# Optimization experiments

Measured on AMD Instinct MI355X. Metric: run time of the kernel, lower is better.

## Reference

```python
import jax, jax.numpy as jnp
import numpy as np

B, T, IN, H = 1024, 128, 5, 100  # batch, seq_len, input_size, hidden_size


def setup_inputs() -> dict:
    key = jax.random.key(0)
    ks = jax.random.split(key, 20)
    bound = 1.0 / np.sqrt(H)  # PyTorch LSTM init: U(-1/sqrt(H), 1/sqrt(H))

    def u(k, shape):
        return jax.random.uniform(k, shape, jnp.float32, -bound, bound)

    inp = {"x": jax.random.normal(ks[0], (B, T, IN), jnp.float32)}
    i = 1
    for layer, din in [(0, IN), (1, 2 * H)]:
        for d in ("f", "b"):
            inp[f"w_ih_l{layer}{d}"] = u(ks[i], (4 * H, din)); i += 1
            inp[f"w_hh_l{layer}{d}"] = u(ks[i], (4 * H, H)); i += 1
            inp[f"b_ih_l{layer}{d}"] = u(ks[i], (4 * H,)); i += 1
            inp[f"b_hh_l{layer}{d}"] = u(ks[i], (4 * H,)); i += 1
    inp["fc_w"] = u(ks[17], (3, 2 * H))
    inp["fc_b"] = u(ks[18], (3,))
    return inp


def _run_dir(x, w_ih, w_hh, b_ih, b_hh, reverse):
    """One LSTM direction. x: [B,T,D] -> hidden seq [B,T,H]. PyTorch gate order i,f,g,o."""
    xT = jnp.swapaxes(x, 0, 1)  # [T,B,D]
    # precompute input contribution for all timesteps: [T,B,4H]
    xg = jnp.einsum('tbd,gd->tbg', xT, w_ih) + b_ih + b_hh

    def step(carry, g_in):
        h, c = carry
        g = g_in + h @ w_hh.T  # [B,4H]
        i, f, gg, o = jnp.split(g, 4, axis=-1)
        c = jax.nn.sigmoid(f) * c + jax.nn.sigmoid(i) * jnp.tanh(gg)
        h = jax.nn.sigmoid(o) * jnp.tanh(c)
        return (h, c), h

    b = x.shape[0]
    init = (jnp.zeros((b, H), x.dtype), jnp.zeros((b, H), x.dtype))
    _, hs = jax.lax.scan(step, init, xg, reverse=reverse)  # hs[t] aligned with time t
    return jnp.swapaxes(hs, 0, 1)  # [B,T,H]


def reference(x,
              w_ih_l0f, w_hh_l0f, b_ih_l0f, b_hh_l0f,
              w_ih_l0b, w_hh_l0b, b_ih_l0b, b_hh_l0b,
              w_ih_l1f, w_hh_l1f, b_ih_l1f, b_hh_l1f,
              w_ih_l1b, w_hh_l1b, b_ih_l1b, b_hh_l1b,
              fc_w, fc_b):
    # Layer 0 (bidirectional): [B,T,2H]
    h0 = jnp.concatenate([
        _run_dir(x, w_ih_l0f, w_hh_l0f, b_ih_l0f, b_hh_l0f, False),
        _run_dir(x, w_ih_l0b, w_hh_l0b, b_ih_l0b, b_hh_l0b, True),
    ], axis=-1)
    # (inter-layer dropout p=0.2 is identity in eval mode)
    # Layer 1 (bidirectional): [B,T,2H]
    h1 = jnp.concatenate([
        _run_dir(h0, w_ih_l1f, w_hh_l1f, b_ih_l1f, b_hh_l1f, False),
        _run_dir(h0, w_ih_l1b, w_hh_l1b, b_ih_l1b, b_hh_l1b, True),
    ], axis=-1)
    last = h1[:, -1, :]  # [B,2H]
    # (dropout p=0.5 is identity in eval mode)
    logits = last @ fc_w.T + fc_b  # [B,3]
    return jax.nn.softmax(logits, axis=1)
```

## Files before the change

kernel.cpp:

```cpp
#include <hip/hip_runtime.h>
#include <hip/hip_fp16.h>


typedef __attribute__((ext_vector_type(8))) short bf16x8;
typedef __attribute__((ext_vector_type(4))) float f32x4;

constexpr int Bsz = 1024, Tt = 128, IN_ = 5, H = 100, G = 400, D1 = 200;
constexpr int NP = 512;
constexpr int NT = 25;
constexpr int MB = 8;
constexpr int MB1 = 4;

__device__ __forceinline__ float sigm(float x)   { return 1.f / (1.f + __expf(-x)); }
__device__ __forceinline__ float tanhf_(float x) { return 1.f - 2.f / (__expf(2.f * x) + 1.f); }
__device__ __forceinline__ unsigned short f2bf(float f) {
  unsigned u = __float_as_uint(f);
  u += 0x7fff + ((u >> 16) & 1);
  return (unsigned short)(u >> 16);
}

__device__ __forceinline__ void pack_body(
    const float* wA, int KA, const float* wB, int KB, int kbo,
    const float* b1, const float* b2, int bias_k,
    unsigned short* dst, int Kg, int idx) {
  if (idx >= Kg * NP * 8) return;
  int jj = idx & 7, rest = idx >> 3;
  int np_ = rest % NP, g = rest / NP;
  int j = np_ >> 2, gate = np_ & 3;
  int k = g * 8 + jj;
  float v = 0.f;
  if (j < H) {
    int n = gate * H + j;
    if (k < KA) v = wA[n * KA + k];
    else if (KB > 0 && k >= kbo && k < kbo + KB) v = wB[n * KB + (k - kbo)];
    else if (k == bias_k) v = b1[n] + b2[n];
  }
  dst[idx] = f2bf(v);
}

__global__ void pack_all(
    const float* __restrict__ w_hh_l0f, const float* __restrict__ w_ih_l0f,
    const float* __restrict__ b_ih_l0f, const float* __restrict__ b_hh_l0f,
    const float* __restrict__ w_hh_l0b, const float* __restrict__ w_ih_l0b,
    const float* __restrict__ b_ih_l0b, const float* __restrict__ b_hh_l0b,
    const float* __restrict__ w_hh_l1f, const float* __restrict__ b_ih_l1f,
    const float* __restrict__ b_hh_l1f,
    const float* __restrict__ w_ih_l1f, const float* __restrict__ w_ih_l1b,
    const float* __restrict__ b_ih_l1b, const float* __restrict__ b_hh_l1b,
    unsigned short* __restrict__ pk0f, unsigned short* __restrict__ pk0b,
    unsigned short* __restrict__ pkhh, unsigned short* __restrict__ pkxg,
    unsigned short* __restrict__ pk1b) {
  int idx = blockIdx.x * 256 + threadIdx.x;
  switch (blockIdx.y) {
    case 0: pack_body(w_hh_l0f, 100, w_ih_l0f, 5, 100, b_ih_l0f, b_hh_l0f, 105, pk0f, 16, idx); break;
    case 1: pack_body(w_hh_l0b, 100, w_ih_l0b, 5, 100, b_ih_l0b, b_hh_l0b, 105, pk0b, 16, idx); break;
    case 2: pack_body(w_hh_l1f, 100, nullptr, 0, 0, b_ih_l1f, b_hh_l1f, -1, pkhh, 16, idx); break;
    case 3: pack_body(w_ih_l1f, 200, nullptr, 0, 0, b_ih_l1f, b_hh_l1f, 200, pkxg, 28, idx); break;
    default: pack_body(w_ih_l1b, 200, nullptr, 0, 0, b_ih_l1b, b_hh_l1b, 200, pk1b, 28, idx);
  }
}

__global__ __launch_bounds__(1024, 1) void lstm_l0(
    const float* __restrict__ x,
    const unsigned short* __restrict__ pk_f, const unsigned short* __restrict__ pk_b,
    unsigned short* __restrict__ h0fT, unsigned short* __restrict__ h0bT) {
  __shared__ __align__(16) short A_s[2][16][16][8];

  const int tid = threadIdx.x;
  const int lane = tid & 63, w = tid >> 6;
  const int q = lane >> 4, l16 = lane & 15;
  const int b0 = blockIdx.x * MB;
  const int dir = blockIdx.y;
  const unsigned short* pk = dir ? pk_b : pk_f;
  unsigned short* hT = dir ? h0bT : h0fT;

  for (int i = tid; i < 2 * 16 * 16 * 8; i += 1024) ((short*)A_s)[i] = 0;

  const int mtA = w, mtB = w + 16;
  const bool bvalid = (mtB < NT);
  bf16x8 wfA[4], wfB[4];
#pragma unroll
  for (int kt = 0; kt < 4; ++kt) {
    wfA[kt] = *(const bf16x8*)(pk + ((size_t)(kt * 4 + q) * NP + mtA * 16 + l16) * 8);
    wfB[kt] = *(const bf16x8*)(pk + ((size_t)(kt * 4 + q) * NP + mtB * 16 + l16) * 8);
  }
  float c = 0.f;
  const bool up = (l16 >= 8);
  const int mm = l16 & 7;
  const int j = (up ? mtB : mtA) * 4 + q;
  const bool valid = up ? bvalid : true;
  const int xm = tid / IN_, xe = tid - xm * IN_;
  const int sm = tid / 25, sj = (tid - (tid / 25) * 25) * 4;
  const float* xp = x + ((size_t)(b0 + xm) * Tt + (dir ? Tt - 2 : 1)) * IN_ + xe;
  const int xstride = dir ? -IN_ : IN_;
  unsigned short* hp =
      hT + ((size_t)(dir ? Tt - 1 : 0) * Bsz + b0 + sm) * H + sj;
  const int hstride = dir ? -(Bsz * H) : (Bsz * H);
  __syncthreads();
  if (tid < 16) {
    A_s[0][13][tid][1] = (short)f2bf(1.f);
    A_s[1][13][tid][1] = (short)f2bf(1.f);
  }
  if (tid < MB * IN_) {
    int t0 = dir ? (Tt - 1) : 0;
    int k = 100 + xe;
    A_s[0][k >> 3][xm][k & 7] =
        (short)f2bf(x[((size_t)(b0 + xm) * Tt + t0) * IN_ + xe]);
  }
  __syncthreads();

  int p = 0;
  for (int step = 0; step < Tt; ++step) {
    if (step > 0 && tid < 200) {
      uint2 hv = *(const uint2*)&A_s[p][sj >> 3][sm][sj & 7];
      *(uint2*)hp = hv;
      hp += hstride;
    }
    float xn = 0.f;
    const bool do_x = (tid < MB * IN_) && (step < Tt - 1);
    if (do_x) { xn = *xp; xp += xstride; }
    bf16x8 hfrag[4];
#pragma unroll
    for (int kt = 0; kt < 4; ++kt) hfrag[kt] = *(const bf16x8*)A_s[p][kt * 4 + q][l16 & 7];
    f32x4 accA = (f32x4){0.f, 0.f, 0.f, 0.f};
    f32x4 accB = (f32x4){0.f, 0.f, 0.f, 0.f};
#pragma unroll
    for (int kt = 0; kt < 4; ++kt)
      accA = __builtin_amdgcn_mfma_f32_16x16x32_bf16(wfA[kt], hfrag[kt], accA, 0, 0, 0);
    if (bvalid) {
#pragma unroll
      for (int kt = 0; kt < 4; ++kt)
        accB = __builtin_amdgcn_mfma_f32_16x16x32_bf16(wfB[kt], hfrag[kt], accB, 0, 0, 0);
    }
    float g0 = up ? accB[0] : accA[0];
    float g1 = up ? accB[1] : accA[1];
    float g2 = up ? accB[2] : accA[2];
    float g3 = up ? accB[3] : accA[3];
    float cc = sigm(g1) * c + sigm(g0) * tanhf_(g2);
    c = cc;
    float h = sigm(g3) * tanhf_(cc);
    if (valid) A_s[1 - p][j >> 3][mm][j & 7] = (short)f2bf(h);
    if (do_x) {
      int k = 100 + xe;
      A_s[1 - p][k >> 3][xm][k & 7] = (short)f2bf(xn);
    }
    __syncthreads();
    p ^= 1;
  }
  if (tid < 200) *(uint2*)hp = *(const uint2*)&A_s[p][sj >> 3][sm][sj & 7];
}

__global__ __launch_bounds__(1024, 1) void gemm_xg(
    const unsigned short* __restrict__ h0fT, const unsigned short* __restrict__ h0bT,
    const unsigned short* __restrict__ pkw, __half* __restrict__ xg) {
  __shared__ __align__(16) short B_s[28][64][8];
  const int tid = threadIdx.x;
  const int lane = tid & 63, w = tid >> 6;
  const int q = lane >> 4, l16 = lane & 15;
  const int r0 = blockIdx.x * 64;
  const size_t base = (size_t)r0 * H;

  for (int i = tid; i < 3 * 64 * 8; i += 1024) {
    int jj = i & 7, gl = i >> 9;
    ((short*)&B_s[25][0][0])[i] = (short)((gl == 0 && jj == 0) ? f2bf(1.f) : 0);
  }
  for (int idx = tid; idx < 1600; idx += 1024) {
    int m = idx / 25, j0 = (idx - (idx / 25) * 25) * 4;
    *(uint2*)&B_s[j0 >> 3][m][j0 & 7] = *(const uint2*)(h0fT + base + m * H + j0);
    int k = 100 + j0;
    *(uint2*)&B_s[k >> 3][m][k & 7] = *(const uint2*)(h0bT + base + m * H + j0);
  }

  const int mtA = w, mtB = w + 16;
  const bool bvalid = (mtB < NT);
  bf16x8 wfA[7], wfB[7];
#pragma unroll
  for (int kt = 0; kt < 7; ++kt) {
    wfA[kt] = *(const bf16x8*)(pkw + ((size_t)(kt * 4 + q) * NP + mtA * 16 + l16) * 8);
    wfB[kt] = *(const bf16x8*)(pkw + ((size_t)(kt * 4 + q) * NP + mtB * 16 + l16) * 8);
  }
  const int jA = mtA * 4 + q, jB = mtB * 4 + q;
  __syncthreads();

#pragma unroll
  for (int rg = 0; rg < 4; ++rg) {
    f32x4 accA = (f32x4){0.f, 0.f, 0.f, 0.f};
    f32x4 accB = (f32x4){0.f, 0.f, 0.f, 0.f};
#pragma unroll
    for (int kt = 0; kt < 7; ++kt) {
      bf16x8 hf = *(const bf16x8*)B_s[kt * 4 + q][rg * 16 + l16];
      accA = __builtin_amdgcn_mfma_f32_16x16x32_bf16(wfA[kt], hf, accA, 0, 0, 0);
      if (bvalid)
        accB = __builtin_amdgcn_mfma_f32_16x16x32_bf16(wfB[kt], hf, accB, 0, 0, 0);
    }
    const size_t row = (size_t)(r0 + rg * 16 + l16);
    {
      __half2 h01 = __floats2half2_rn(accA[0], accA[1]);
      __half2 h23 = __floats2half2_rn(accA[2], accA[3]);
      uint2 st; *(__half2*)&st.x = h01; *(__half2*)&st.y = h23;
      *(uint2*)(xg + row * G + 4 * jA) = st;
    }
    if (bvalid) {
      __half2 h01 = __floats2half2_rn(accB[0], accB[1]);
      __half2 h23 = __floats2half2_rn(accB[2], accB[3]);
      uint2 st; *(__half2*)&st.x = h01; *(__half2*)&st.y = h23;
      *(uint2*)(xg + row * G + 4 * jB) = st;
    }
  }
}

__global__ __launch_bounds__(1024, 1) void lstm_l1(
    const unsigned short* __restrict__ h0fT, const unsigned short* __restrict__ h0bT,
    const unsigned short* __restrict__ pk_hh, const unsigned short* __restrict__ pk1b,
    const __half* __restrict__ xg,
    const float* __restrict__ fc_w, const float* __restrict__ fc_b,
    float* __restrict__ out) {
  __shared__ __align__(16) short A_s[2][16][16][8];
  __shared__ __align__(16) short A2_s[28][16][8];
  __shared__ float hf_s[MB1][H];
  __shared__ float hb_s[MB1][H];
  __shared__ float fcw_s[3 * D1];
  __shared__ float fcb_s[3];
  __shared__ float logit_s[MB1][3];

  const int tid = threadIdx.x;
  const int lane = tid & 63, w = tid >> 6;
  const int q = lane >> 4, l16 = lane & 15;
  const int b0 = blockIdx.x * MB1;
  const uint2* xg2 = (const uint2*)xg;

  for (int i = tid; i < 2 * 16 * 16 * 8; i += 1024) ((short*)A_s)[i] = 0;
  for (int i = tid; i < 25 * 16 * 8; i += 1024) ((short*)A2_s)[i] = 0;
  for (int i = tid; i < 3 * 16 * 8; i += 1024) {
    int jj = i & 7, gl = i >> 7;
    ((short*)&A2_s[25][0][0])[i] = (short)((gl == 0 && jj == 0) ? f2bf(1.f) : 0);
  }
  for (int i = tid; i < 3 * D1; i += 1024) fcw_s[i] = fc_w[i];
  if (tid < 3) fcb_s[tid] = fc_b[tid];

  const bool busy = (w < 7);
  const int m = l16 & 3, g16 = l16 >> 2;
  const int myMt = w * 4 + g16;
  const int jme = myMt * 4 + q;
  const bool evalid = busy && (myMt < NT);
  int mts[4]; bool tv[4];
  bf16x8 wf[4][4];
  if (busy) {
#pragma unroll
    for (int i = 0; i < 4; ++i) {
      int mt = w * 4 + i; mts[i] = mt; tv[i] = (mt < NT);
#pragma unroll
      for (int kt = 0; kt < 4; ++kt)
        wf[i][kt] = *(const bf16x8*)(pk_hh + ((size_t)(kt * 4 + q) * NP + mt * 16 + l16) * 8);
    }
  }
  float c = 0.f;
  const uint2* xgp = xg2 + (size_t)(b0 + m) * 100 + jme;
  uint2 xgCur = {0, 0};
  if (busy) { xgCur = *xgp; xgp += Bsz * 100; }
  __syncthreads();

  int p = 0;
  for (int t = 0; t < Tt; ++t) {
    if (busy) {
      uint2 xgNxt = xgCur;
      if (t < Tt - 1) { xgNxt = *xgp; xgp += Bsz * 100; }
      bf16x8 hfrag[4];
#pragma unroll
      for (int kt = 0; kt < 4; ++kt) hfrag[kt] = *(const bf16x8*)A_s[p][kt * 4 + q][l16 & 3];
      f32x4 acc[4];
#pragma unroll
      for (int i = 0; i < 4; ++i) {
        acc[i] = (f32x4){0.f, 0.f, 0.f, 0.f};
        if (!tv[i]) continue;
#pragma unroll
        for (int kt = 0; kt < 4; ++kt)
          acc[i] = __builtin_amdgcn_mfma_f32_16x16x32_bf16(wf[i][kt], hfrag[kt], acc[i], 0, 0, 0);
      }
      float2 x01 = __half22float2(*(const __half2*)&xgCur.x);
      float2 x23 = __half22float2(*(const __half2*)&xgCur.y);
      float xr[4] = {x01.x, x01.y, x23.x, x23.y};
      float gr[4];
#pragma unroll
      for (int r = 0; r < 4; ++r) {
        float lo = (g16 & 1) ? acc[1][r] : acc[0][r];
        float hi = (g16 & 1) ? acc[3][r] : acc[2][r];
        gr[r] = ((g16 & 2) ? hi : lo) + xr[r];
      }
      float cc = sigm(gr[1]) * c + sigm(gr[0]) * tanhf_(gr[2]);
      c = cc;
      float h = sigm(gr[3]) * tanhf_(cc);
      if (evalid) {
        A_s[1 - p][jme >> 3][m][jme & 7] = (short)f2bf(h);
        if (t == Tt - 1) hf_s[m][jme] = h;
      }
      xgCur = xgNxt;
    }
    __syncthreads();
    p ^= 1;
  }

  {
    const size_t base = ((size_t)(Tt - 1) * Bsz + b0) * H;
    if (tid < 100) {
      int m2 = tid / 25, j0 = (tid - (tid / 25) * 25) * 4;
      *(uint2*)&A2_s[j0 >> 3][m2][j0 & 7] = *(const uint2*)(h0fT + base + m2 * H + j0);
      int k = 100 + j0;
      *(uint2*)&A2_s[k >> 3][m2][k & 7] = *(const uint2*)(h0bT + base + m2 * H + j0);
    }
  }
  __syncthreads();
  if (busy) {
    f32x4 acc[4];
#pragma unroll
    for (int i = 0; i < 4; ++i) acc[i] = (f32x4){0.f, 0.f, 0.f, 0.f};
#pragma unroll
    for (int kt = 0; kt < 7; ++kt) {
      bf16x8 hf = *(const bf16x8*)A2_s[kt * 4 + q][l16 & 3];
#pragma unroll
      for (int i = 0; i < 4; ++i) {
        if (!tv[i]) continue;
        bf16x8 wfb = *(const bf16x8*)(pk1b + ((size_t)(kt * 4 + q) * NP + mts[i] * 16 + l16) * 8);
        acc[i] = __builtin_amdgcn_mfma_f32_16x16x32_bf16(wfb, hf, acc[i], 0, 0, 0);
      }
    }
    float gr[4];
#pragma unroll
    for (int r = 0; r < 4; ++r) {
      float lo = (g16 & 1) ? acc[1][r] : acc[0][r];
      float hi = (g16 & 1) ? acc[3][r] : acc[2][r];
      gr[r] = (g16 & 2) ? hi : lo;
    }
    float cc = sigm(gr[0]) * tanhf_(gr[2]);
    if (evalid) hb_s[m][jme] = sigm(gr[3]) * tanhf_(cc);
  }
  __syncthreads();

  if (tid < MB1 * 3) {
    int mr = tid / 3, cls = tid - mr * 3;
    float s = fcb_s[cls];
    for (int jj = 0; jj < H; ++jj) s += fcw_s[cls * D1 + jj] * hf_s[mr][jj];
    for (int jj = 0; jj < H; ++jj) s += fcw_s[cls * D1 + H + jj] * hb_s[mr][jj];
    logit_s[mr][cls] = s;
  }
  __syncthreads();
  if (tid < MB1) {
    float a = logit_s[tid][0], b = logit_s[tid][1], cc = logit_s[tid][2];
    float mx = fmaxf(a, fmaxf(b, cc));
    float e0 = __expf(a - mx), e1 = __expf(b - mx), e2 = __expf(cc - mx);
    float inv = 1.f / (e0 + e1 + e2);
    out[(b0 + tid) * 3 + 0] = e0 * inv;
    out[(b0 + tid) * 3 + 1] = e1 * inv;
    out[(b0 + tid) * 3 + 2] = e2 * inv;
  }
}

extern "C" void kernel_launch(void* const* d_in, const int* in_sizes, int n_in,
                              void* d_out, int out_size, void* d_ws, size_t ws_size,
                              hipStream_t stream) {
  const float* x        = (const float*)d_in[0];
  const float* w_ih_l0f = (const float*)d_in[1];
  const float* w_hh_l0f = (const float*)d_in[2];
  const float* b_ih_l0f = (const float*)d_in[3];
  const float* b_hh_l0f = (const float*)d_in[4];
  const float* w_ih_l0b = (const float*)d_in[5];
  const float* w_hh_l0b = (const float*)d_in[6];
  const float* b_ih_l0b = (const float*)d_in[7];
  const float* b_hh_l0b = (const float*)d_in[8];
  const float* w_ih_l1f = (const float*)d_in[9];
  const float* w_hh_l1f = (const float*)d_in[10];
  const float* b_ih_l1f = (const float*)d_in[11];
  const float* b_hh_l1f = (const float*)d_in[12];
  const float* w_ih_l1b = (const float*)d_in[13];
  const float* b_ih_l1b = (const float*)d_in[15];
  const float* b_hh_l1b = (const float*)d_in[16];
  const float* fc_w     = (const float*)d_in[17];
  const float* fc_b     = (const float*)d_in[18];

  unsigned short* h0fT = (unsigned short*)d_ws;
  unsigned short* h0bT = h0fT + (size_t)Tt * Bsz * H;
  __half* xgT          = (__half*)(h0bT + (size_t)Tt * Bsz * H);
  unsigned short* pk0f = (unsigned short*)(xgT + (size_t)Tt * Bsz * G);
  unsigned short* pk0b = pk0f + 16 * NP * 8;
  unsigned short* pkhh = pk0b + 16 * NP * 8;
  unsigned short* pkxg = pkhh + 16 * NP * 8;
  unsigned short* pk1b = pkxg + 28 * NP * 8;

  pack_all<<<dim3(448, 5), 256, 0, stream>>>(
      w_hh_l0f, w_ih_l0f, b_ih_l0f, b_hh_l0f,
      w_hh_l0b, w_ih_l0b, b_ih_l0b, b_hh_l0b,
      w_hh_l1f, b_ih_l1f, b_hh_l1f,
      w_ih_l1f, w_ih_l1b, b_ih_l1b, b_hh_l1b,
      pk0f, pk0b, pkhh, pkxg, pk1b);

  lstm_l0<<<dim3(Bsz / MB, 2), 1024, 0, stream>>>(x, pk0f, pk0b, h0fT, h0bT);
  gemm_xg<<<(Bsz * Tt) / 64, 1024, 0, stream>>>(h0fT, h0bT, pkxg, xgT);
  lstm_l1<<<Bsz / MB1, 1024, 0, stream>>>(h0fT, h0bT, pkhh, pk1b, xgT,
                                          fc_w, fc_b, (float*)d_out);
}
```

Baseline: 375.8 us.

## Make gemm_xg persistent with double-buffered LDS prefetch; replicate h rows in LSTM LDS

The input-projection GEMM now launches 512 blocks, and each block processes four 64-row groups. The next group's h0 tiles are loaded into registers while MFMAs run on the current LDS buffer, which amortises the weight-fragment loads and hides global-load latency. Both LSTM recurrence kernels now write each h value into replicated LDS rows, so the fragment read indexes by l16 instead of l16&7 or l16&3. This is likely meant to avoid LDS broadcast bank conflicts, at the cost of extra LDS stores on the serial critical path. The GEMM also adds a double LDS buffer and runs with fewer blocks in flight.

```diff
diff --git a/kernel.cpp b/kernel.cpp
--- a/kernel.cpp
+++ b/kernel.cpp
@@ -10,6 +10,8 @@
 constexpr int NT = 25;
 constexpr int MB = 8;
 constexpr int MB1 = 4;
+constexpr int NGRP = 4;
+constexpr int GSTRIDE = 512;
 
 __device__ __forceinline__ float sigm(float x)   { return 1.f / (1.f + __expf(-x)); }
 __device__ __forceinline__ float tanhf_(float x) { return 1.f - 2.f / (__expf(2.f * x) + 1.f); }
@@ -104,8 +106,9 @@
   if (tid < MB * IN_) {
     int t0 = dir ? (Tt - 1) : 0;
     int k = 100 + xe;
-    A_s[0][k >> 3][xm][k & 7] =
-        (short)f2bf(x[((size_t)(b0 + xm) * Tt + t0) * IN_ + xe]);
+    short xv = (short)f2bf(x[((size_t)(b0 + xm) * Tt + t0) * IN_ + xe]);
+    A_s[0][k >> 3][xm][k & 7] = xv;
+    A_s[0][k >> 3][xm + 8][k & 7] = xv;
   }
   __syncthreads();
 
@@ -121,7 +124,7 @@
     if (do_x) { xn = *xp; xp += xstride; }
     bf16x8 hfrag[4];
 #pragma unroll
-    for (int kt = 0; kt < 4; ++kt) hfrag[kt] = *(const bf16x8*)A_s[p][kt * 4 + q][l16 & 7];
+    for (int kt = 0; kt < 4; ++kt) hfrag[kt] = *(const bf16x8*)A_s[p][kt * 4 + q][l16];
     f32x4 accA = (f32x4){0.f, 0.f, 0.f, 0.f};
     f32x4 accB = (f32x4){0.f, 0.f, 0.f, 0.f};
 #pragma unroll
@@ -139,10 +142,16 @@
     float cc = sigm(g1) * c + sigm(g0) * tanhf_(g2);
     c = cc;
     float h = sigm(g3) * tanhf_(cc);
-    if (valid) A_s[1 - p][j >> 3][mm][j & 7] = (short)f2bf(h);
+    if (valid) {
+      short hh = (short)f2bf(h);
+      A_s[1 - p][j >> 3][mm][j & 7] = hh;
+      A_s[1 - p][j >> 3][mm + 8][j & 7] = hh;
+    }
     if (do_x) {
       int k = 100 + xe;
-      A_s[1 - p][k >> 3][xm][k & 7] = (short)f2bf(xn);
+      short xv = (short)f2bf(xn);
+      A_s[1 - p][k >> 3][xm][k & 7] = xv;
+      A_s[1 - p][k >> 3][xm + 8][k & 7] = xv;
     }
     __syncthreads();
     p ^= 1;
@@ -153,23 +162,17 @@
 __global__ __launch_bounds__(1024, 1) void gemm_xg(
     const unsigned short* __restrict__ h0fT, const unsigned short* __restrict__ h0bT,
     const unsigned short* __restrict__ pkw, __half* __restrict__ xg) {
-  __shared__ __align__(16) short B_s[28][64][8];
+  __shared__ __align__(16) short B_s[2][28][64][8];
   const int tid = threadIdx.x;
   const int lane = tid & 63, w = tid >> 6;
   const int q = lane >> 4, l16 = lane & 15;
-  const int r0 = blockIdx.x * 64;
-  const size_t base = (size_t)r0 * H;
-
-  for (int i = tid; i < 3 * 64 * 8; i += 1024) {
-    int jj = i & 7, gl = i >> 9;
-    ((short*)&B_s[25][0][0])[i] = (short)((gl == 0 && jj == 0) ? f2bf(1.f) : 0);
-  }
-  for (int idx = tid; idx < 1600; idx += 1024) {
-    int m = idx / 25, j0 = (idx - (idx / 25) * 25) * 4;
-    *(uint2*)&B_s[j0 >> 3][m][j0 & 7] = *(const uint2*)(h0fT + base + m * H + j0);
-    int k = 100 + j0;
-    *(uint2*)&B_s[k >> 3][m][k & 7] = *(const uint2*)(h0bT + base + m * H + j0);
-  }
+
+#pragma unroll
+  for (int b = 0; b < 2; ++b)
+    for (int i = tid; i < 3 * 64 * 8; i += 1024) {
+      int jj = i & 7, gl = i >> 9;
+      ((short*)&B_s[b][25][0][0])[i] = (short)((gl == 0 && jj == 0) ? f2bf(1.f) : 0);
+    }
 
   const int mtA = w, mtB = w + 16;
   const bool bvalid = (mtB < NT);
@@ -180,33 +183,73 @@
     wfB[kt] = *(const bf16x8*)(pkw + ((size_t)(kt * 4 + q) * NP + mtB * 16 + l16) * 8);
   }
   const int jA = mtA * 4 + q, jB = mtB * 4 + q;
-  __syncthreads();
-
-#pragma unroll
-  for (int rg = 0; rg < 4; ++rg) {
-    f32x4 accA = (f32x4){0.f, 0.f, 0.f, 0.f};
-    f32x4 accB = (f32x4){0.f, 0.f, 0.f, 0.f};
-#pragma unroll
-    for (int kt = 0; kt < 7; ++kt) {
-      bf16x8 hf = *(const bf16x8*)B_s[kt * 4 + q][rg * 16 + l16];
-      accA = __builtin_amdgcn_mfma_f32_16x16x32_bf16(wfA[kt], hf, accA, 0, 0, 0);
-      if (bvalid)
-        accB = __builtin_amdgcn_mfma_f32_16x16x32_bf16(wfB[kt], hf, accB, 0, 0, 0);
-    }
-    const size_t row = (size_t)(r0 + rg * 16 + l16);
-    {
-      __half2 h01 = __floats2half2_rn(accA[0], accA[1]);
-      __half2 h23 = __floats2half2_rn(accA[2], accA[3]);
-      uint2 st; *(__half2*)&st.x = h01; *(__half2*)&st.y = h23;
-      *(uint2*)(xg + row * G + 4 * jA) = st;
-    }
-    if (bvalid) {
-      __half2 h01 = __floats2half2_rn(accB[0], accB[1]);
-      __half2 h23 = __floats2half2_rn(accB[2], accB[3]);
-      uint2 st; *(__half2*)&st.x = h01; *(__half2*)&st.y = h23;
-      *(uint2*)(xg + row * G + 4 * jB) = st;
-    }
-  }
+
+  const int t0m = tid / 25, t0j = (tid - t0m * 25) * 4;
+  const int t1 = tid + 1024;
+  const int t1m = t1 / 25, t1j = (t1 - t1m * 25) * 4;
+  uint2 sf0, sb0, sf1, sb1;
+
+#define XG_ISSUE(GRP)                                                  \
+  {                                                                    \
+    size_t base_ = (size_t)(GRP)*64 * H;                               \
+    sf0 = *(const uint2*)(h0fT + base_ + t0m * H + t0j);               \
+    sb0 = *(const uint2*)(h0bT + base_ + t0m * H + t0j);               \
+    if (tid < 576) {                                                   \
+      sf1 = *(const uint2*)(h0fT + base_ + t1m * H + t1j);             \
+      sb1 = *(const uint2*)(h0bT + base_ + t1m * H + t1j);             \
+    }                                                                  \
+  }
+#define XG_COMMIT(BUF)                                                 \
+  {                                                                    \
+    *(uint2*)&B_s[BUF][t0j >> 3][t0m][t0j & 7] = sf0;                  \
+    int k0_ = 100 + t0j;                                               \
+    *(uint2*)&B_s[BUF][k0_ >> 3][t0m][k0_ & 7] = sb0;                  \
+    if (tid < 576) {                                                   \
+      *(uint2*)&B_s[BUF][t1j >> 3][t1m][t1j & 7] = sf1;                \
+      int k1_ = 100 + t1j;                                             \
+      *(uint2*)&B_s[BUF][k1_ >> 3][t1m][k1_ & 7] = sb1;                \
+    }                                                                  \
+  }
+
+  const int g0 = blockIdx.x;
+  XG_ISSUE(g0);
+  XG_COMMIT(0);
+  __syncthreads();
+
+  for (int i = 0; i < NGRP; ++i) {
+    if (i < NGRP - 1) XG_ISSUE(g0 + GSTRIDE * (i + 1));
+    const short(*Bb)[64][8] = B_s[i & 1];
+    const int r0 = (g0 + GSTRIDE * i) * 64;
+#pragma unroll
+    for (int rg = 0; rg < 4; ++rg) {
+      f32x4 accA = (f32x4){0.f, 0.f, 0.f, 0.f};
+      f32x4 accB = (f32x4){0.f, 0.f, 0.f, 0.f};
+#pragma unroll
+      for (int kt = 0; kt < 7; ++kt) {
+        bf16x8 hf = *(const bf16x8*)Bb[kt * 4 + q][rg * 16 + l16];
+        accA = __builtin_amdgcn_mfma_f32_16x16x32_bf16(wfA[kt], hf, accA, 0, 0, 0);
+        if (bvalid)
+          accB = __builtin_amdgcn_mfma_f32_16x16x32_bf16(wfB[kt], hf, accB, 0, 0, 0);
+      }
+      const size_t row = (size_t)(r0 + rg * 16 + l16);
+      {
+        __half2 h01 = __floats2half2_rn(accA[0], accA[1]);
+        __half2 h23 = __floats2half2_rn(accA[2], accA[3]);
+        uint2 st; *(__half2*)&st.x = h01; *(__half2*)&st.y = h23;
+        *(uint2*)(xg + row * G + 4 * jA) = st;
+      }
+      if (bvalid) {
+        __half2 h01 = __floats2half2_rn(accB[0], accB[1]);
+        __half2 h23 = __floats2half2_rn(accB[2], accB[3]);
+        uint2 st; *(__half2*)&st.x = h01; *(__half2*)&st.y = h23;
+        *(uint2*)(xg + row * G + 4 * jB) = st;
+      }
+    }
+    if (i < NGRP - 1) XG_COMMIT((i & 1) ^ 1);
+    __syncthreads();
+  }
+#undef XG_ISSUE
+#undef XG_COMMIT
 }
 
 __global__ __launch_bounds__(1024, 1) void lstm_l1(
@@ -267,7 +310,7 @@
       if (t < Tt - 1) { xgNxt = *xgp; xgp += Bsz * 100; }
       bf16x8 hfrag[4];
 #pragma unroll
-      for (int kt = 0; kt < 4; ++kt) hfrag[kt] = *(const bf16x8*)A_s[p][kt * 4 + q][l16 & 3];
+      for (int kt = 0; kt < 4; ++kt) hfrag[kt] = *(const bf16x8*)A_s[p][kt * 4 + q][l16];
       f32x4 acc[4];
 #pragma unroll
       for (int i = 0; i < 4; ++i) {
@@ -291,7 +334,11 @@
       c = cc;
       float h = sigm(gr[3]) * tanhf_(cc);
       if (evalid) {
-        A_s[1 - p][jme >> 3][m][jme & 7] = (short)f2bf(h);
+        short hh = (short)f2bf(h);
+        A_s[1 - p][jme >> 3][m][jme & 7] = hh;
+        A_s[1 - p][jme >> 3][m + 4][jme & 7] = hh;
+        A_s[1 - p][jme >> 3][m + 8][jme & 7] = hh;
+        A_s[1 - p][jme >> 3][m + 12][jme & 7] = hh;
         if (t == Tt - 1) hf_s[m][jme] = h;
       }
       xgCur = xgNxt;
@@ -394,7 +441,7 @@
       pk0f, pk0b, pkhh, pkxg, pk1b);
 
   lstm_l0<<<dim3(Bsz / MB, 2), 1024, 0, stream>>>(x, pk0f, pk0b, h0fT, h0bT);
-  gemm_xg<<<(Bsz * Tt) / 64, 1024, 0, stream>>>(h0fT, h0bT, pkxg, xgT);
+  gemm_xg<<<GSTRIDE, 1024, 0, stream>>>(h0fT, h0bT, pkxg, xgT);
   lstm_l1<<<Bsz / MB1, 1024, 0, stream>>>(h0fT, h0bT, pkhh, pk1b, xgT,
                                           fc_w, fc_b, (float*)d_out);
 }
```

New measurement: 358.4 us. -4.6%, faster.
